# Performance work log

Hardware: AMD Instinct MI355X
Metric: run time of the kernel (lower is better)

The kernel has to match this reference:

```python
import jax, jax.numpy as jnp
import numpy as np

B, RES, DIM, H, KD = 16, 32, 768, 12, 64
N = RES * RES          # 1024 tokens
D = KD                 # attn_ratio = 1 -> per-head value dim == key_dim
DH = D * H             # 768
SCALE = KD ** -0.5
LN_EPS = 1e-5


def _bias_idxs():
    # replicate the itertools.product construction: for row-major points,
    # offsets (|dy|,|dx|) are first seen in order dy-major, so id = |dy|*RES + |dx|
    coords = np.arange(N)
    y, x = coords // RES, coords % RES
    dy = np.abs(y[:, None] - y[None, :])
    dx = np.abs(x[:, None] - x[None, :])
    return jnp.asarray(dy * RES + dx, dtype=jnp.int32)  # [N, N]


def setup_inputs() -> dict:
    key = jax.random.key(0)
    ks = jax.random.split(key, 8)
    return {
        "x": jax.random.normal(ks[0], (B, N, DIM), jnp.float32),
        "ln_w": 1.0 + 0.01 * jax.random.normal(ks[1], (DIM,), jnp.float32),
        "ln_b": 0.01 * jax.random.normal(ks[2], (DIM,), jnp.float32),
        "qkv_w": 0.02 * jax.random.normal(ks[3], (3 * H * KD, DIM), jnp.float32),
        "qkv_b": 0.01 * jax.random.normal(ks[4], (3 * H * KD,), jnp.float32),
        "proj_w": 0.02 * jax.random.normal(ks[5], (DIM, DH), jnp.float32),
        "proj_b": 0.01 * jax.random.normal(ks[6], (DIM,), jnp.float32),
        "attn_biases": 0.1 * jax.random.normal(ks[7], (H, RES * RES), jnp.float32),
        "bias_idxs": _bias_idxs(),
    }


def reference(x, ln_w, ln_b, qkv_w, qkv_b, proj_w, proj_b, attn_biases, bias_idxs):
    # LayerNorm over the feature dim
    mu = jnp.mean(x, axis=-1, keepdims=True)
    var = jnp.mean(jnp.square(x - mu), axis=-1, keepdims=True)
    xn = (x - mu) * jax.lax.rsqrt(var + LN_EPS) * ln_w + ln_b

    # fused qkv projection -> [B, N, H, 3*KD], split per head
    qkv = (xn @ qkv_w.T + qkv_b).reshape(B, N, H, 3 * KD)
    q, k, v = jnp.split(qkv, [KD, 2 * KD], axis=3)  # each [B, N, H, KD]

    # gathered relative-position bias: [H, N, N]
    bias = attn_biases[:, bias_idxs]

    # scores + bias -> softmax -> AV
    attn = jnp.einsum("bnhk,bmhk->bhnm", q, k) * SCALE + bias[None]
    attn = jax.nn.softmax(attn, axis=-1)
    out = jnp.einsum("bhnm,bmhd->bnhd", attn, v).reshape(B, N, DH)
    return out @ proj_w.T + proj_b
```

## Files before the change

### kernel.cpp

```cpp
#include <hip/hip_runtime.h>
#include <cstdint>
#include <cstddef>

#define AS1 __attribute__((address_space(1)))
#define AS3 __attribute__((address_space(3)))

typedef float f32x4 __attribute__((ext_vector_type(4)));
typedef __bf16 bf16x8 __attribute__((ext_vector_type(8)));
typedef __bf16 bf16x4 __attribute__((ext_vector_type(4)));
typedef _Float16 h16x4 __attribute__((ext_vector_type(4)));
typedef uint32_t u32x4 __attribute__((ext_vector_type(4)));

__device__ __forceinline__ void async_cp16(void* lds, const void* g) {
    __builtin_amdgcn_global_load_lds((AS1 void*)(g), (AS3 void*)(lds), 16, 0, 0);
}

__device__ __forceinline__ bf16x8 frag_of(u32x4 u) {
    return __builtin_bit_cast(bf16x8, u);
}

__global__ __launch_bounds__(256)
void cvt_w(const float* __restrict__ qkvw, const float* __restrict__ projw,
           __bf16* __restrict__ qkvwb, __bf16* __restrict__ projwb) {
    int i = blockIdx.x * 256 + threadIdx.x;
    if (i < 442368) {
        int row = i / 192, c4 = (i - row * 192) * 4;
        int t = (row >= 1536) ? 2 : (row >= 768 ? 1 : 0);
        int rem = row - t * 768;
        int hh = rem >> 6, d = rem & 63;
        int in_row = hh * 192 + t * 64 + d;
        float4 v = *(const float4*)(qkvw + (long)in_row * 768 + c4);
        bf16x4 o;
        o[0] = (__bf16)v.x; o[1] = (__bf16)v.y; o[2] = (__bf16)v.z; o[3] = (__bf16)v.w;
        *(bf16x4*)(qkvwb + (long)row * 768 + c4) = o;
    } else {
        int j = i - 442368;
        float4 v = ((const float4*)projw)[j];
        bf16x4 o;
        o[0] = (__bf16)v.x; o[1] = (__bf16)v.y; o[2] = (__bf16)v.z; o[3] = (__bf16)v.w;
        ((bf16x4*)projwb)[j] = o;
    }
}

__global__ __launch_bounds__(256)
void ln_kernel(const float* __restrict__ x, const float* __restrict__ w,
               const float* __restrict__ bsh, __bf16* __restrict__ xn) {
    const int lane = threadIdx.x & 63;
    const long row = (long)blockIdx.x * 4 + (threadIdx.x >> 6);
    const float4* xr = (const float4*)(x + row * 768);
    float4 v[3];
    v[0] = xr[lane]; v[1] = xr[lane + 64]; v[2] = xr[lane + 128];
    float s = 0.f, ss = 0.f;
#pragma unroll
    for (int i = 0; i < 3; ++i) {
        s  += v[i].x + v[i].y + v[i].z + v[i].w;
        ss += v[i].x * v[i].x + v[i].y * v[i].y + v[i].z * v[i].z + v[i].w * v[i].w;
    }
#pragma unroll
    for (int m = 1; m < 64; m <<= 1) { s += __shfl_xor(s, m); ss += __shfl_xor(ss, m); }
    const float mean = s * (1.f / 768.f);
    const float rstd = rsqrtf(ss * (1.f / 768.f) - mean * mean + 1e-5f);
    const float4* wv = (const float4*)w;
    const float4* bv = (const float4*)bsh;
    bf16x4* outp = (bf16x4*)(xn + row * 768);
#pragma unroll
    for (int i = 0; i < 3; ++i) {
        float4 wi = wv[lane + 64 * i], bi = bv[lane + 64 * i];
        bf16x4 o;
        o[0] = (__bf16)((v[i].x - mean) * rstd * wi.x + bi.x);
        o[1] = (__bf16)((v[i].y - mean) * rstd * wi.y + bi.y);
        o[2] = (__bf16)((v[i].z - mean) * rstd * wi.z + bi.z);
        o[3] = (__bf16)((v[i].w - mean) * rstd * wi.w + bi.w);
        outp[lane + 64 * i] = o;
    }
}

template <int MODE>
__device__ __forceinline__
void gemm_core(__bf16* As, __bf16* Bs,
               const __bf16* __restrict__ A, const __bf16* __restrict__ Bw,
               const float* __restrict__ bias,
               __bf16* __restrict__ q_out, __bf16* __restrict__ k_out,
               __bf16* __restrict__ vt_out, float* __restrict__ f_out,
               long bm, long bn) {
    constexpr int K = 768;
    const int tid  = threadIdx.x;
    const int lane = tid & 63;
    const int quad = lane >> 4;
    const int l16  = lane & 15;
    const int wave = tid >> 6;
    const int wm = wave >> 1, wn = wave & 1;

    const __bf16* Ab = A  + bm * K;
    const __bf16* Bb = Bw + bn * K;

    const int el0 = tid, el1 = tid + 256;
    const int rA0 = el0 >> 2, rA1 = el1 >> 2;
    const int kc  = (tid & 3) * 8;

    f32x4 acc[4][4] = {};

    for (int k0 = 0; k0 < K; k0 += 32) {
        __syncthreads();
        async_cp16((char*)As + el0 * 16, Ab + (long)rA0 * K + (k0 + kc));
        async_cp16((char*)As + el1 * 16, Ab + (long)rA1 * K + (k0 + kc));
        async_cp16((char*)Bs + el0 * 16, Bb + (long)rA0 * K + (k0 + kc));
        async_cp16((char*)Bs + el1 * 16, Bb + (long)rA1 * K + (k0 + kc));
        __syncthreads();

        const u32x4* Av = (const u32x4*)As;
        const u32x4* Bv = (const u32x4*)Bs;
        bf16x8 af[4], bfr[4];
#pragma unroll
        for (int t = 0; t < 4; ++t) {
            af[t]  = frag_of(Av[(wm * 64 + t * 16 + l16) * 4 + quad]);
            bfr[t] = frag_of(Bv[(wn * 64 + t * 16 + l16) * 4 + quad]);
        }
#pragma unroll
        for (int i = 0; i < 4; ++i)
#pragma unroll
            for (int j = 0; j < 4; ++j) {
                if constexpr (MODE == 0)
                    acc[i][j] = __builtin_amdgcn_mfma_f32_16x16x32_bf16(bfr[j], af[i], acc[i][j], 0, 0, 0);
                else
                    acc[i][j] = __builtin_amdgcn_mfma_f32_16x16x32_bf16(af[i], bfr[j], acc[i][j], 0, 0, 0);
            }
    }

    if constexpr (MODE == 0) {
#pragma unroll
        for (int j = 0; j < 4; ++j) {
            int col0 = (int)bn + wn * 64 + j * 16 + quad * 4;
            int t  = col0 >= 768;
            int cc = col0 - t * 768;
            int h  = cc >> 6, d = cc & 63;
            int f  = h * 192 + t * 64 + d;
            float4 bb = *(const float4*)(bias + f);
            __bf16* dst = t ? k_out : q_out;
#pragma unroll
            for (int i = 0; i < 4; ++i) {
                long row = bm + wm * 64 + i * 16 + l16;
                long b   = row >> 10;
                long n   = row & 1023;
                bf16x4 pk;
                pk[0] = (__bf16)(acc[i][j][0] + bb.x);
                pk[1] = (__bf16)(acc[i][j][1] + bb.y);
                pk[2] = (__bf16)(acc[i][j][2] + bb.z);
                pk[3] = (__bf16)(acc[i][j][3] + bb.w);
                *(bf16x4*)(dst + ((b * 12 + h) * 1024 + n) * 64 + d) = pk;
            }
        }
    } else if constexpr (MODE == 2) {
#pragma unroll
        for (int j = 0; j < 4; ++j) {
            int cv = (int)bn - 1536 + wn * 64 + j * 16 + l16;
            int h  = cv >> 6, d = cv & 63;
            float bv = bias[h * 192 + 128 + d];
#pragma unroll
            for (int i = 0; i < 4; ++i) {
                long row0 = bm + wm * 64 + i * 16 + quad * 4;
                long b    = row0 >> 10;
                long n0   = row0 & 1023;
                bf16x4 pk;
                pk[0] = (__bf16)(acc[i][j][0] + bv);
                pk[1] = (__bf16)(acc[i][j][1] + bv);
                pk[2] = (__bf16)(acc[i][j][2] + bv);
                pk[3] = (__bf16)(acc[i][j][3] + bv);
                *(bf16x4*)(vt_out + ((b * 12 + h) * 64 + d) * 1024 + n0) = pk;
            }
        }
    } else {
#pragma unroll
        for (int i = 0; i < 4; ++i) {
#pragma unroll
            for (int r = 0; r < 4; ++r) {
                long row = bm + wm * 64 + i * 16 + quad * 4 + r;
#pragma unroll
                for (int j = 0; j < 4; ++j) {
                    int col = (int)bn + wn * 64 + j * 16 + l16;
                    f_out[row * 768 + col] = acc[i][j][r] + bias[col];
                }
            }
        }
    }
}

__global__ __launch_bounds__(256, 3)
void gemm_qkv(const __bf16* __restrict__ A, const __bf16* __restrict__ Bw,
              const float* __restrict__ bias, __bf16* __restrict__ qb,
              __bf16* __restrict__ kb, __bf16* __restrict__ vtb) {
    __shared__ __align__(16) __bf16 As[128 * 32];
    __shared__ __align__(16) __bf16 Bs[128 * 32];
    int blk  = blockIdx.x;
    int xcd  = blk & 7;
    int rest = blk >> 3;
    int bx   = rest % 18;
    int byg  = rest / 18;
    long by  = xcd + 8 * byg;
    if (bx < 12)
        gemm_core<0>(As, Bs, A, Bw, bias, qb, kb, nullptr, nullptr, by * 128, (long)bx * 128);
    else
        gemm_core<2>(As, Bs, A, Bw, bias, nullptr, nullptr, vtb, nullptr, by * 128, (long)bx * 128);
}

__global__ __launch_bounds__(256, 3)
void gemm_proj(const __bf16* __restrict__ A, const __bf16* __restrict__ Bw,
               const float* __restrict__ bias, float* __restrict__ out) {
    __shared__ __align__(16) __bf16 As[128 * 32];
    __shared__ __align__(16) __bf16 Bs[128 * 32];
    int blk  = blockIdx.x;
    int xcd  = blk & 7;
    int rest = blk >> 3;
    int bx   = rest % 6;
    int byg  = rest / 6;
    long by  = xcd + 8 * byg;
    gemm_core<1>(As, Bs, A, Bw, bias, nullptr, nullptr, nullptr, out,
                 by * 128, (long)bx * 128);
}

__global__ __launch_bounds__(512, 6)
void attn_kernel(const __bf16* __restrict__ Q, const __bf16* __restrict__ Kb,
                 const __bf16* __restrict__ Vt, const float* __restrict__ biases,
                 __bf16* __restrict__ out) {
    __shared__ __align__(16) __bf16 QPs[128 * 64];
    __shared__ __align__(16) __bf16 Ks[2][64 * 64];
    __shared__ __align__(16) __bf16 Vts[2][64 * 64];
    __shared__ __align__(16) float brow[1024];

    const int tid  = threadIdx.x;
    const int lane = tid & 63;
    const int wave = tid >> 6;
    const int quad = lane >> 4;
    const int l16  = lane & 15;
    const int sw   = l16 & 7;

    int blk  = blockIdx.x;
    int xcd  = blk & 7;
    int rest = blk >> 3;
    int qt   = rest & 7;
    int bhg  = rest >> 3;
    int bh_i = xcd + 8 * bhg;
    int b    = bh_i / 12;
    int h    = bh_i - b * 12;

    const long bh = bh_i;
    const __bf16* Qg  = Q  + (bh * 1024 + qt * 128) * 64;
    const __bf16* Kg  = Kb + bh * 1024 * 64;
    const __bf16* Vtg = Vt + bh * 64 * 1024;

    {
        const int e0 = tid, e1 = tid + 512;
        const int r0 = e0 >> 3, c0 = (e0 & 7) ^ (r0 & 7);
        const int r1 = e1 >> 3, c1 = (e1 & 7) ^ (r1 & 7);
        async_cp16((char*)QPs + e0 * 16, Qg + r0 * 64 + c0 * 8);
        async_cp16((char*)QPs + e1 * 16, Qg + r1 * 64 + c1 * 8);
    }
    const int rk = tid >> 3;
    const int ck = (tid & 7) ^ (rk & 7);
    async_cp16((char*)Ks[0]  + tid * 16, Kg  + rk * 64   + ck * 8);
    async_cp16((char*)Vts[0] + tid * 16, Vtg + rk * 1024 + ck * 8);
    {
        const float LOG2E = 1.4426950408889634f;
        float2 v = ((const float2*)(biases + (long)h * 1024))[tid];
        float2 o; o.x = v.x * LOG2E; o.y = v.y * LOG2E;
        *(float2*)(brow + tid * 2) = o;
    }
    __syncthreads();

    bf16x8 aq[2];
    {
        const u32x4* Qv = (const u32x4*)QPs;
        int qrow = wave * 16 + l16;
        aq[0] = frag_of(Qv[qrow * 8 + (quad ^ sw)]);
        aq[1] = frag_of(Qv[qrow * 8 + ((quad + 4) ^ sw)]);
    }

    const int yq = 4 * qt + (wave >> 1);
    const int xq = ((wave & 1) << 4) + l16;
    int pdx[2][4];
#pragma unroll
    for (int i2 = 0; i2 < 2; ++i2)
#pragma unroll
        for (int r = 0; r < 4; ++r) {
            int xk = (i2 << 4) + quad * 4 + r;
            int d = xq - xk; pdx[i2][r] = d < 0 ? -d : d;
        }

    const float SSCALE = 0.125f * 1.4426950408889634f;
    float lacc = 0.f;
    f32x4 o[4] = {};
    __bf16* Psw = QPs + wave * 1024;
    const int pwb = l16 * 128 + (quad & 1) * 8;

    for (int kt = 0; kt < 16; ++kt) {
        const int cb = kt & 1;
        if (kt < 15) {
            const int nb = cb ^ 1;
            const __bf16* Kt  = Kg  + (kt + 1) * 4096;
            const __bf16* Vtt = Vtg + (kt + 1) * 64;
            async_cp16((char*)Ks[nb]  + tid * 16, Kt  + rk * 64   + ck * 8);
            async_cp16((char*)Vts[nb] + tid * 16, Vtt + rk * 1024 + ck * 8);
        }

        f32x4 s[4];
        const u32x4* Kv = (const u32x4*)Ks[cb];
#pragma unroll
        for (int nt = 0; nt < 4; ++nt) {
            int krow = nt * 16 + l16;
            bf16x8 k0 = frag_of(Kv[krow * 8 + (quad ^ sw)]);
            bf16x8 k1 = frag_of(Kv[krow * 8 + ((quad + 4) ^ sw)]);
            f32x4 z = {0.f, 0.f, 0.f, 0.f};
            z = __builtin_amdgcn_mfma_f32_16x16x32_bf16(k0, aq[0], z, 0, 0, 0);
            z = __builtin_amdgcn_mfma_f32_16x16x32_bf16(k1, aq[1], z, 0, 0, 0);
            s[nt] = z;
        }

        int dy0 = yq - 2 * kt;     dy0 = dy0 < 0 ? -dy0 : dy0;
        int dy1 = yq - 2 * kt - 1; dy1 = dy1 < 0 ? -dy1 : dy1;
        const float* br0 = brow + dy0 * 32;
        const float* br1 = brow + dy1 * 32;
#pragma unroll
        for (int nt = 0; nt < 4; ++nt) {
            const float* br = (nt & 2) ? br1 : br0;
            bf16x4 pk;
#pragma unroll
            for (int r = 0; r < 4; ++r) {
                float p = __builtin_amdgcn_exp2f(s[nt][r] * SSCALE + br[pdx[nt & 1][r]]);
                lacc += p;
                pk[r] = (__bf16)p;
            }
            *(bf16x4*)((char*)Psw + pwb + (((nt * 2 + (quad >> 1)) ^ sw) << 4)) = pk;
        }

        const u32x4* Pv = (const u32x4*)Psw;
        const u32x4* Vv = (const u32x4*)Vts[cb];
        bf16x8 bp0 = frag_of(Pv[l16 * 8 + (quad ^ sw)]);
        bf16x8 bp1 = frag_of(Pv[l16 * 8 + ((quad + 4) ^ sw)]);
#pragma unroll
        for (int dt = 0; dt < 4; ++dt) {
            int vrow = dt * 16 + l16;
            bf16x8 v0 = frag_of(Vv[vrow * 8 + (quad ^ sw)]);
            bf16x8 v1 = frag_of(Vv[vrow * 8 + ((quad + 4) ^ sw)]);
            o[dt] = __builtin_amdgcn_mfma_f32_16x16x32_bf16(v0, bp0, o[dt], 0, 0, 0);
            o[dt] = __builtin_amdgcn_mfma_f32_16x16x32_bf16(v1, bp1, o[dt], 0, 0, 0);
        }

        __syncthreads();
    }

    lacc += __shfl_xor(lacc, 16);
    lacc += __shfl_xor(lacc, 32);
    const float rl = 1.f / lacc;

    const long n = qt * 128 + wave * 16 + l16;
    __bf16* op = out + ((long)b * 1024 + n) * 768 + h * 64 + quad * 4;
#pragma unroll
    for (int dt = 0; dt < 4; ++dt) {
        bf16x4 ov;
        ov[0] = (__bf16)(o[dt][0] * rl);
        ov[1] = (__bf16)(o[dt][1] * rl);
        ov[2] = (__bf16)(o[dt][2] * rl);
        ov[3] = (__bf16)(o[dt][3] * rl);
        *(bf16x4*)(op + dt * 16) = ov;
    }
}

extern "C" void kernel_launch(void* const* d_in, const int* in_sizes, int n_in,
                              void* d_out, int out_size, void* d_ws, size_t ws_size,
                              hipStream_t stream) {
    (void)in_sizes; (void)n_in; (void)out_size; (void)ws_size;
    const float* x      = (const float*)d_in[0];
    const float* ln_w   = (const float*)d_in[1];
    const float* ln_b   = (const float*)d_in[2];
    const float* qkv_w  = (const float*)d_in[3];
    const float* qkv_b  = (const float*)d_in[4];
    const float* proj_w = (const float*)d_in[5];
    const float* proj_b = (const float*)d_in[6];
    const float* ab     = (const float*)d_in[7];
    float* outp = (float*)d_out;

    char* ws = (char*)d_ws;
    __bf16* xn     = (__bf16*)(ws);
    __bf16* aout   = (__bf16*)(ws);
    __bf16* qkvwb  = (__bf16*)(ws + 25165824);
    __bf16* projwb = (__bf16*)(ws + 28704768);
    __bf16* qb     = (__bf16*)(ws + 29884416);
    __bf16* kb     = (__bf16*)(ws + 55050240);
    __bf16* vtb    = (__bf16*)(ws + 80216064);

    cvt_w<<<2304, 256, 0, stream>>>(qkv_w, proj_w, qkvwb, projwb);
    ln_kernel<<<4096, 256, 0, stream>>>(x, ln_w, ln_b, xn);
    gemm_qkv<<<2304, 256, 0, stream>>>(xn, qkvwb, qkv_b, qb, kb, vtb);
    attn_kernel<<<1536, 512, 0, stream>>>(qb, kb, vtb, ab, aout);
    gemm_proj<<<768, 256, 0, stream>>>(aout, projwb, proj_b, outp);
}
```

Baseline: 311.0 us.

## Triple-buffer GEMM K loop and keep attention P in registers with 32 rows per wave

The shared GEMM core now uses a three-stage LDS ring with async global-to-LDS copies, partial vmcnt waits, an XOR swizzle against bank conflicts, and raised wave priority around the MFMA block. This overlaps loads with compute and drops one barrier per K step. The attention kernel moves from 512 to 256 threads, each wave owning 32 query rows. Softmax probabilities are packed straight into MFMA operand registers instead of round-tripping through LDS, and V fragments are gathered to match that layout. The cost is higher register pressure, 48KB of LDS per GEMM block, and less occupancy in attention.

```diff
diff --git a/kernel.cpp b/kernel.cpp
--- a/kernel.cpp
+++ b/kernel.cpp
@@ -8,7 +8,6 @@
 typedef float f32x4 __attribute__((ext_vector_type(4)));
 typedef __bf16 bf16x8 __attribute__((ext_vector_type(8)));
 typedef __bf16 bf16x4 __attribute__((ext_vector_type(4)));
-typedef _Float16 h16x4 __attribute__((ext_vector_type(4)));
 typedef uint32_t u32x4 __attribute__((ext_vector_type(4)));
 
 __device__ __forceinline__ void async_cp16(void* lds, const void* g) {
@@ -77,7 +76,7 @@
 
 template <int MODE>
 __device__ __forceinline__
-void gemm_core(__bf16* As, __bf16* Bs,
+void gemm_core(char* smem,
                const __bf16* __restrict__ A, const __bf16* __restrict__ Bw,
                const float* __restrict__ bias,
                __bf16* __restrict__ q_out, __bf16* __restrict__ k_out,
@@ -94,28 +93,33 @@
     const __bf16* Ab = A  + bm * K;
     const __bf16* Bb = Bw + bn * K;
 
-    const int el0 = tid, el1 = tid + 256;
-    const int rA0 = el0 >> 2, rA1 = el1 >> 2;
-    const int kc  = (tid & 3) * 8;
+    const int e0 = tid, e1 = tid + 256;
+    const int rA0 = e0 >> 2, c0 = ((e0 & 3) ^ ((e0 >> 3) & 3)) * 8;
+    const int rA1 = e1 >> 2, c1 = ((e1 & 3) ^ ((e1 >> 3) & 3)) * 8;
+    const int swq = quad ^ ((l16 >> 1) & 3);
 
     f32x4 acc[4][4] = {};
 
-    for (int k0 = 0; k0 < K; k0 += 32) {
-        __syncthreads();
-        async_cp16((char*)As + el0 * 16, Ab + (long)rA0 * K + (k0 + kc));
-        async_cp16((char*)As + el1 * 16, Ab + (long)rA1 * K + (k0 + kc));
-        async_cp16((char*)Bs + el0 * 16, Bb + (long)rA0 * K + (k0 + kc));
-        async_cp16((char*)Bs + el1 * 16, Bb + (long)rA1 * K + (k0 + kc));
-        __syncthreads();
-
-        const u32x4* Av = (const u32x4*)As;
-        const u32x4* Bv = (const u32x4*)Bs;
+    auto stage = [&](int t) {
+        char* base = smem + (t % 3) * 16384;
+        const __bf16* As_ = Ab + t * 32;
+        const __bf16* Bs_ = Bb + t * 32;
+        async_cp16(base + e0 * 16,        As_ + (long)rA0 * K + c0);
+        async_cp16(base + e1 * 16,        As_ + (long)rA1 * K + c1);
+        async_cp16(base + 8192 + e0 * 16, Bs_ + (long)rA0 * K + c0);
+        async_cp16(base + 8192 + e1 * 16, Bs_ + (long)rA1 * K + c1);
+    };
+
+    auto kstep = [&](int buf) {
+        const u32x4* Av = (const u32x4*)(smem + buf * 16384);
+        const u32x4* Bv = (const u32x4*)(smem + buf * 16384 + 8192);
         bf16x8 af[4], bfr[4];
 #pragma unroll
         for (int t = 0; t < 4; ++t) {
-            af[t]  = frag_of(Av[(wm * 64 + t * 16 + l16) * 4 + quad]);
-            bfr[t] = frag_of(Bv[(wn * 64 + t * 16 + l16) * 4 + quad]);
-        }
+            af[t]  = frag_of(Av[(wm * 64 + t * 16 + l16) * 4 + swq]);
+            bfr[t] = frag_of(Bv[(wn * 64 + t * 16 + l16) * 4 + swq]);
+        }
+        __builtin_amdgcn_s_setprio(1);
 #pragma unroll
         for (int i = 0; i < 4; ++i)
 #pragma unroll
@@ -125,7 +129,19 @@
                 else
                     acc[i][j] = __builtin_amdgcn_mfma_f32_16x16x32_bf16(af[i], bfr[j], acc[i][j], 0, 0, 0);
             }
-    }
+        __builtin_amdgcn_s_setprio(0);
+    };
+
+    stage(0); stage(1);
+    for (int t = 0; t < 23; ++t) {
+        asm volatile("s_waitcnt vmcnt(4)" ::: "memory");
+        __builtin_amdgcn_s_barrier();
+        if (t < 22) stage(t + 2);
+        kstep(t % 3);
+    }
+    asm volatile("s_waitcnt vmcnt(0)" ::: "memory");
+    __builtin_amdgcn_s_barrier();
+    kstep(23 % 3);
 
     if constexpr (MODE == 0) {
 #pragma unroll
@@ -189,8 +205,7 @@
 void gemm_qkv(const __bf16* __restrict__ A, const __bf16* __restrict__ Bw,
               const float* __restrict__ bias, __bf16* __restrict__ qb,
               __bf16* __restrict__ kb, __bf16* __restrict__ vtb) {
-    __shared__ __align__(16) __bf16 As[128 * 32];
-    __shared__ __align__(16) __bf16 Bs[128 * 32];
+    __shared__ __align__(16) char smem[49152];
     int blk  = blockIdx.x;
     int xcd  = blk & 7;
     int rest = blk >> 3;
@@ -198,31 +213,29 @@
     int byg  = rest / 18;
     long by  = xcd + 8 * byg;
     if (bx < 12)
-        gemm_core<0>(As, Bs, A, Bw, bias, qb, kb, nullptr, nullptr, by * 128, (long)bx * 128);
+        gemm_core<0>(smem, A, Bw, bias, qb, kb, nullptr, nullptr, by * 128, (long)bx * 128);
     else
-        gemm_core<2>(As, Bs, A, Bw, bias, nullptr, nullptr, vtb, nullptr, by * 128, (long)bx * 128);
+        gemm_core<2>(smem, A, Bw, bias, nullptr, nullptr, vtb, nullptr, by * 128, (long)bx * 128);
 }
 
 __global__ __launch_bounds__(256, 3)
 void gemm_proj(const __bf16* __restrict__ A, const __bf16* __restrict__ Bw,
                const float* __restrict__ bias, float* __restrict__ out) {
-    __shared__ __align__(16) __bf16 As[128 * 32];
-    __shared__ __align__(16) __bf16 Bs[128 * 32];
+    __shared__ __align__(16) char smem[49152];
     int blk  = blockIdx.x;
     int xcd  = blk & 7;
     int rest = blk >> 3;
     int bx   = rest % 6;
     int byg  = rest / 6;
     long by  = xcd + 8 * byg;
-    gemm_core<1>(As, Bs, A, Bw, bias, nullptr, nullptr, nullptr, out,
+    gemm_core<1>(smem, A, Bw, bias, nullptr, nullptr, nullptr, out,
                  by * 128, (long)bx * 128);
 }
 
-__global__ __launch_bounds__(512, 6)
+__global__ __launch_bounds__(256, 4)
 void attn_kernel(const __bf16* __restrict__ Q, const __bf16* __restrict__ Kb,
                  const __bf16* __restrict__ Vt, const float* __restrict__ biases,
                  __bf16* __restrict__ out) {
-    __shared__ __align__(16) __bf16 QPs[128 * 64];
     __shared__ __align__(16) __bf16 Ks[2][64 * 64];
     __shared__ __align__(16) __bf16 Vts[2][64 * 64];
     __shared__ __align__(16) float brow[1024];
@@ -248,49 +261,57 @@
     const __bf16* Kg  = Kb + bh * 1024 * 64;
     const __bf16* Vtg = Vt + bh * 64 * 1024;
 
-    {
-        const int e0 = tid, e1 = tid + 512;
-        const int r0 = e0 >> 3, c0 = (e0 & 7) ^ (r0 & 7);
-        const int r1 = e1 >> 3, c1 = (e1 & 7) ^ (r1 & 7);
-        async_cp16((char*)QPs + e0 * 16, Qg + r0 * 64 + c0 * 8);
-        async_cp16((char*)QPs + e1 * 16, Qg + r1 * 64 + c1 * 8);
-    }
     const int rk = tid >> 3;
     const int ck = (tid & 7) ^ (rk & 7);
-    async_cp16((char*)Ks[0]  + tid * 16, Kg  + rk * 64   + ck * 8);
-    async_cp16((char*)Vts[0] + tid * 16, Vtg + rk * 1024 + ck * 8);
+
     {
         const float LOG2E = 1.4426950408889634f;
-        float2 v = ((const float2*)(biases + (long)h * 1024))[tid];
-        float2 o; o.x = v.x * LOG2E; o.y = v.y * LOG2E;
-        *(float2*)(brow + tid * 2) = o;
-    }
+        float4 v = ((const float4*)(biases + (long)h * 1024))[tid];
+        float4 o; o.x = v.x * LOG2E; o.y = v.y * LOG2E;
+        o.z = v.z * LOG2E; o.w = v.w * LOG2E;
+        *(float4*)(brow + tid * 4) = o;
+    }
+#pragma unroll
+    for (int j = 0; j < 4; ++j) {
+        int e = tid + 256 * j;
+        int r = e >> 3, c = (e & 7) ^ (r & 7);
+        async_cp16((char*)Vts + e * 16, Qg + r * 64 + c * 8);
+    }
+    async_cp16((char*)Ks[0] + tid * 16,         Kg + rk * 64 + ck * 8);
+    async_cp16((char*)Ks[0] + (tid + 256) * 16, Kg + (rk + 32) * 64 + ck * 8);
     __syncthreads();
 
-    bf16x8 aq[2];
+    bf16x8 aq[2][2];
     {
-        const u32x4* Qv = (const u32x4*)QPs;
-        int qrow = wave * 16 + l16;
-        aq[0] = frag_of(Qv[qrow * 8 + (quad ^ sw)]);
-        aq[1] = frag_of(Qv[qrow * 8 + ((quad + 4) ^ sw)]);
-    }
-
-    const int yq = 4 * qt + (wave >> 1);
-    const int xq = ((wave & 1) << 4) + l16;
-    int pdx[2][4];
-#pragma unroll
-    for (int i2 = 0; i2 < 2; ++i2)
-#pragma unroll
-        for (int r = 0; r < 4; ++r) {
-            int xk = (i2 << 4) + quad * 4 + r;
-            int d = xq - xk; pdx[i2][r] = d < 0 ? -d : d;
-        }
+        const u32x4* Qv = (const u32x4*)Vts;
+#pragma unroll
+        for (int g = 0; g < 2; ++g) {
+            int qrow = wave * 32 + g * 16 + l16;
+            aq[g][0] = frag_of(Qv[qrow * 8 + (quad ^ sw)]);
+            aq[g][1] = frag_of(Qv[qrow * 8 + ((quad + 4) ^ sw)]);
+        }
+    }
+    __syncthreads();
+    async_cp16((char*)Vts[0] + tid * 16,         Vtg + rk * 1024 + ck * 8);
+    async_cp16((char*)Vts[0] + (tid + 256) * 16, Vtg + (rk + 32) * 1024 + ck * 8);
+    __syncthreads();
+
+    const int yq = 4 * qt + wave;
+    int pdx00[4], pdx01[4], pdx10[4];
+#pragma unroll
+    for (int r = 0; r < 4; ++r) {
+        int xk = quad * 4 + r;
+        int d0 = l16 - xk;
+        pdx00[r] = d0 < 0 ? -d0 : d0;
+        pdx01[r] = 16 - d0;
+        pdx10[r] = 16 + d0;
+    }
 
     const float SSCALE = 0.125f * 1.4426950408889634f;
-    float lacc = 0.f;
-    f32x4 o[4] = {};
-    __bf16* Psw = QPs + wave * 1024;
-    const int pwb = l16 * 128 + (quad & 1) * 8;
+    float lacc[2] = {0.f, 0.f};
+    f32x4 o[2][4] = {};
+    const int q2 = quad >> 1;
+    const int hb = (quad & 1) * 8;
 
     for (int kt = 0; kt < 16; ++kt) {
         const int cb = kt & 1;
@@ -298,70 +319,89 @@
             const int nb = cb ^ 1;
             const __bf16* Kt  = Kg  + (kt + 1) * 4096;
             const __bf16* Vtt = Vtg + (kt + 1) * 64;
-            async_cp16((char*)Ks[nb]  + tid * 16, Kt  + rk * 64   + ck * 8);
-            async_cp16((char*)Vts[nb] + tid * 16, Vtt + rk * 1024 + ck * 8);
-        }
-
-        f32x4 s[4];
+            async_cp16((char*)Ks[nb]  + tid * 16,         Kt  + rk * 64 + ck * 8);
+            async_cp16((char*)Ks[nb]  + (tid + 256) * 16, Kt  + (rk + 32) * 64 + ck * 8);
+            async_cp16((char*)Vts[nb] + tid * 16,         Vtt + rk * 1024 + ck * 8);
+            async_cp16((char*)Vts[nb] + (tid + 256) * 16, Vtt + (rk + 32) * 1024 + ck * 8);
+        }
+
+        f32x4 s[2][4];
         const u32x4* Kv = (const u32x4*)Ks[cb];
 #pragma unroll
         for (int nt = 0; nt < 4; ++nt) {
             int krow = nt * 16 + l16;
             bf16x8 k0 = frag_of(Kv[krow * 8 + (quad ^ sw)]);
             bf16x8 k1 = frag_of(Kv[krow * 8 + ((quad + 4) ^ sw)]);
-            f32x4 z = {0.f, 0.f, 0.f, 0.f};
-            z = __builtin_amdgcn_mfma_f32_16x16x32_bf16(k0, aq[0], z, 0, 0, 0);
-            z = __builtin_amdgcn_mfma_f32_16x16x32_bf16(k1, aq[1], z, 0, 0, 0);
-            s[nt] = z;
+#pragma unroll
+            for (int g = 0; g < 2; ++g) {
+                f32x4 z = {0.f, 0.f, 0.f, 0.f};
+                z = __builtin_amdgcn_mfma_f32_16x16x32_bf16(k0, aq[g][0], z, 0, 0, 0);
+                z = __builtin_amdgcn_mfma_f32_16x16x32_bf16(k1, aq[g][1], z, 0, 0, 0);
+                s[g][nt] = z;
+            }
         }
 
         int dy0 = yq - 2 * kt;     dy0 = dy0 < 0 ? -dy0 : dy0;
         int dy1 = yq - 2 * kt - 1; dy1 = dy1 < 0 ? -dy1 : dy1;
         const float* br0 = brow + dy0 * 32;
         const float* br1 = brow + dy1 * 32;
-#pragma unroll
-        for (int nt = 0; nt < 4; ++nt) {
-            const float* br = (nt & 2) ? br1 : br0;
-            bf16x4 pk;
-#pragma unroll
-            for (int r = 0; r < 4; ++r) {
-                float p = __builtin_amdgcn_exp2f(s[nt][r] * SSCALE + br[pdx[nt & 1][r]]);
-                lacc += p;
-                pk[r] = (__bf16)p;
-            }
-            *(bf16x4*)((char*)Psw + pwb + (((nt * 2 + (quad >> 1)) ^ sw) << 4)) = pk;
-        }
-
-        const u32x4* Pv = (const u32x4*)Psw;
-        const u32x4* Vv = (const u32x4*)Vts[cb];
-        bf16x8 bp0 = frag_of(Pv[l16 * 8 + (quad ^ sw)]);
-        bf16x8 bp1 = frag_of(Pv[l16 * 8 + ((quad + 4) ^ sw)]);
+
+        bf16x8 bpA[2], bpB[2];
+#pragma unroll
+        for (int g = 0; g < 2; ++g) {
+#pragma unroll
+            for (int nt = 0; nt < 4; ++nt) {
+                const float* br = (nt & 2) ? br1 : br0;
+#pragma unroll
+                for (int r = 0; r < 4; ++r) {
+                    int idx = (nt & 1) ? (g ? pdx00[r] : pdx01[r])
+                                       : (g ? pdx10[r] : pdx00[r]);
+                    float p = __builtin_amdgcn_exp2f(s[g][nt][r] * SSCALE + br[idx]);
+                    lacc[g] += p;
+                    if (nt < 2) bpA[g][(nt & 1) * 4 + r] = (__bf16)p;
+                    else        bpB[g][(nt & 1) * 4 + r] = (__bf16)p;
+                }
+            }
+        }
+
+        const char* Vb = (const char*)Vts[cb];
 #pragma unroll
         for (int dt = 0; dt < 4; ++dt) {
-            int vrow = dt * 16 + l16;
-            bf16x8 v0 = frag_of(Vv[vrow * 8 + (quad ^ sw)]);
-            bf16x8 v1 = frag_of(Vv[vrow * 8 + ((quad + 4) ^ sw)]);
-            o[dt] = __builtin_amdgcn_mfma_f32_16x16x32_bf16(v0, bp0, o[dt], 0, 0, 0);
-            o[dt] = __builtin_amdgcn_mfma_f32_16x16x32_bf16(v1, bp1, o[dt], 0, 0, 0);
+            int rb = (dt * 16 + l16) * 128 + hb;
+            uint2 alo = *(const uint2*)(Vb + rb + (((q2    ) ^ sw) << 4));
+            uint2 ahi = *(const uint2*)(Vb + rb + (((q2 + 2) ^ sw) << 4));
+            uint2 blo = *(const uint2*)(Vb + rb + (((q2 + 4) ^ sw) << 4));
+            uint2 bhi = *(const uint2*)(Vb + rb + (((q2 + 6) ^ sw) << 4));
+            u32x4 va = {alo.x, alo.y, ahi.x, ahi.y};
+            u32x4 vbk = {blo.x, blo.y, bhi.x, bhi.y};
+            bf16x8 vA = frag_of(va), vB = frag_of(vbk);
+#pragma unroll
+            for (int g = 0; g < 2; ++g) {
+                o[g][dt] = __builtin_amdgcn_mfma_f32_16x16x32_bf16(vA, bpA[g], o[g][dt], 0, 0, 0);
+                o[g][dt] = __builtin_amdgcn_mfma_f32_16x16x32_bf16(vB, bpB[g], o[g][dt], 0, 0, 0);
+            }
         }
 
         __syncthreads();
     }
 
-    lacc += __shfl_xor(lacc, 16);
-    lacc += __shfl_xor(lacc, 32);
-    const float rl = 1.f / lacc;
-
-    const long n = qt * 128 + wave * 16 + l16;
-    __bf16* op = out + ((long)b * 1024 + n) * 768 + h * 64 + quad * 4;
-#pragma unroll
-    for (int dt = 0; dt < 4; ++dt) {
-        bf16x4 ov;
-        ov[0] = (__bf16)(o[dt][0] * rl);
-        ov[1] = (__bf16)(o[dt][1] * rl);
-        ov[2] = (__bf16)(o[dt][2] * rl);
-        ov[3] = (__bf16)(o[dt][3] * rl);
-        *(bf16x4*)(op + dt * 16) = ov;
+#pragma unroll
+    for (int g = 0; g < 2; ++g) {
+        float la = lacc[g];
+        la += __shfl_xor(la, 16);
+        la += __shfl_xor(la, 32);
+        const float rl = 1.f / la;
+        const long n = qt * 128 + wave * 32 + g * 16 + l16;
+        __bf16* op = out + ((long)b * 1024 + n) * 768 + h * 64 + quad * 4;
+#pragma unroll
+        for (int dt = 0; dt < 4; ++dt) {
+            bf16x4 ov;
+            ov[0] = (__bf16)(o[g][dt][0] * rl);
+            ov[1] = (__bf16)(o[g][dt][1] * rl);
+            ov[2] = (__bf16)(o[g][dt][2] * rl);
+            ov[3] = (__bf16)(o[g][dt][3] * rl);
+            *(bf16x4*)(op + dt * 16) = ov;
+        }
     }
 }
 
@@ -391,6 +431,6 @@
     cvt_w<<<2304, 256, 0, stream>>>(qkv_w, proj_w, qkvwb, projwb);
     ln_kernel<<<4096, 256, 0, stream>>>(x, ln_w, ln_b, xn);
     gemm_qkv<<<2304, 256, 0, stream>>>(xn, qkvwb, qkv_b, qb, kb, vtb);
-    attn_kernel<<<1536, 512, 0, stream>>>(qb, kb, vtb, ab, aout);
+    attn_kernel<<<1536, 256, 0, stream>>>(qb, kb, vtb, ab, aout);
     gemm_proj<<<768, 256, 0, stream>>>(aout, projwb, proj_b, outp);
 }
```

After: 323.7 us. 4.1% more time.
